# Optimization experiments

Hardware: AMD Instinct MI355X
Metric: run time of the kernel (lower is better)

## Reference

```python
import jax, jax.numpy as jnp
import numpy as np

DIM = 768
NH = 12
HD = DIM // NH
MLP = 4 * DIM
EPS = 1e-5


def _ln(x, w, b):
    mu = x.mean(-1, keepdims=True)
    var = ((x - mu) ** 2).mean(-1, keepdims=True)
    return (x - mu) * jax.lax.rsqrt(var + EPS) * w + b


def setup_inputs() -> dict:
    key = jax.random.key(0)
    ks = jax.random.split(key, 12)
    s = 0.02
    return {
        "xq": jax.random.normal(ks[0], (4, 32, 32, DIM), jnp.float32),
        "xkv": jax.random.normal(ks[1], (4, 64, 64, DIM), jnp.float32),
        "norm1_w": jnp.ones((DIM,), jnp.float32),
        "norm1_b": jnp.zeros((DIM,), jnp.float32),
        "kv_w": jax.random.normal(ks[2], (DIM, 2 * DIM), jnp.float32) * s,
        "kv_b": jnp.zeros((2 * DIM,), jnp.float32),
        "q_w": jax.random.normal(ks[3], (DIM, DIM), jnp.float32) * s,
        "q_b": jnp.zeros((DIM,), jnp.float32),
        "proj_w": jax.random.normal(ks[4], (DIM, DIM), jnp.float32) * s,
        "proj_b": jnp.zeros((DIM,), jnp.float32),
        "norm2_w": jnp.ones((DIM,), jnp.float32),
        "norm2_b": jnp.zeros((DIM,), jnp.float32),
        "mlp_w1": jax.random.normal(ks[5], (DIM, MLP), jnp.float32) * s,
        "mlp_b1": jnp.zeros((MLP,), jnp.float32),
        "mlp_w2": jax.random.normal(ks[6], (MLP, DIM), jnp.float32) * s,
        "mlp_b2": jnp.zeros((DIM,), jnp.float32),
    }


def reference(xq, xkv, norm1_w, norm1_b, kv_w, kv_b, q_w, q_b, proj_w, proj_b,
              norm2_w, norm2_b, mlp_w1, mlp_b1, mlp_w2, mlp_b2):
    B, Hq, Wq, C = xq.shape
    _, H, W, _ = xkv.shape
    shortcut = xq
    xn = _ln(xq, norm1_w, norm1_b)
    # kv projection: [B, H*W, 2, NH, HD]
    kv = (xkv.reshape(B, H * W, C) @ kv_w + kv_b).reshape(B, H * W, 2, NH, HD)
    k = kv[:, :, 0].transpose(0, 2, 1, 3)  # [B, NH, HW, HD]
    v = kv[:, :, 1].transpose(0, 2, 1, 3)
    q = (xn.reshape(B, Hq * Wq, C) @ q_w + q_b).reshape(B, Hq * Wq, NH, HD).transpose(0, 2, 1, 3)
    scale = HD ** -0.5
    attn = jnp.einsum('bhqd,bhkd->bhqk', q * scale, k)
    attn = jax.nn.softmax(attn, axis=-1)
    o = jnp.einsum('bhqk,bhkd->bhqd', attn, v)  # [B, NH, HqWq, HD]
    o = o.transpose(0, 2, 1, 3).reshape(B, Hq, Wq, C)
    o = o @ proj_w + proj_b
    x = shortcut + o
    xn2 = _ln(x, norm2_w, norm2_b)
    mlp = jax.nn.gelu(xn2 @ mlp_w1 + mlp_b1, approximate=False) @ mlp_w2 + mlp_b2
    return x + mlp
```

## Files before the change

kernel.cpp:

```cpp
#include <hip/hip_runtime.h>
#include <hip/hip_bf16.h>
#include <math.h>

#define DIM 768
#define NH 12
#define HD 64
#define NQ 1024
#define NKV 4096
#define QSCALE 0.18033688011112042f

typedef __attribute__((ext_vector_type(4))) float f32x4;
typedef __attribute__((ext_vector_type(8))) __bf16 bf16x8;
typedef __attribute__((ext_vector_type(8))) unsigned short u16x8;
typedef __attribute__((ext_vector_type(4))) unsigned short u16x4;
typedef unsigned short u16;

typedef const __attribute__((address_space(1))) void* gas_t;
typedef __attribute__((address_space(3))) void* las_t;

__device__ __forceinline__ void gl16(const void* g, void* l) {
    __builtin_amdgcn_global_load_lds((gas_t)g, (las_t)l, 16, 0, 0);
}

__device__ __forceinline__ u16 f2b(float x) {
    __bf16 h = (__bf16)x;
    return __builtin_bit_cast(u16, h);
}

__device__ __forceinline__ float b2f(u16 x) {
    unsigned int u = ((unsigned int)x) << 16;
    return __builtin_bit_cast(float, u);
}

__device__ __forceinline__ f32x4 mfma16(const u16* a, const u16* b, f32x4 c) {
    bf16x8 av = *reinterpret_cast<const bf16x8*>(a);
    bf16x8 bv = *reinterpret_cast<const bf16x8*>(b);
    return __builtin_amdgcn_mfma_f32_16x16x32_bf16(av, bv, c, 0, 0, 0);
}

__device__ __forceinline__ f32x4 mfmaf(bf16x8 a, bf16x8 b, f32x4 c) {
    return __builtin_amdgcn_mfma_f32_16x16x32_bf16(a, b, c, 0, 0, 0);
}

__device__ __forceinline__ bf16x8 cat44(u16x4 a, u16x4 b) {
    u16x8 r = __builtin_shufflevector(a, b, 0, 1, 2, 3, 4, 5, 6, 7);
    return __builtin_bit_cast(bf16x8, r);
}

__global__ __launch_bounds__(256) void cast_bf16_kernel(
    const float* __restrict__ in, u16* __restrict__ out, int n8)
{
    int i = blockIdx.x * 256 + threadIdx.x;
    if (i >= n8) return;
    const float4* p = reinterpret_cast<const float4*>(in) + (size_t)i * 2;
    float4 a = p[0], b = p[1];
    u16x8 o;
    o[0] = f2b(a.x); o[1] = f2b(a.y); o[2] = f2b(a.z); o[3] = f2b(a.w);
    o[4] = f2b(b.x); o[5] = f2b(b.y); o[6] = f2b(b.z); o[7] = f2b(b.w);
    reinterpret_cast<u16x8*>(out)[i] = o;
}

__global__ __launch_bounds__(256) void transpose_cast_kernel(
    const float* __restrict__ W, u16* __restrict__ Wt, int K, int N)
{
    __shared__ u16 T[64][72];
    int k0 = blockIdx.y * 64, n0 = blockIdx.x * 64;
    int tid = threadIdx.x;
    int r = tid >> 2, c = (tid & 3) * 16;
    const float* src = W + (size_t)(k0 + r) * N + n0 + c;
    #pragma unroll
    for (int j = 0; j < 16; j += 4) {
        float4 f = *reinterpret_cast<const float4*>(src + j);
        T[r][c + j + 0] = f2b(f.x); T[r][c + j + 1] = f2b(f.y);
        T[r][c + j + 2] = f2b(f.z); T[r][c + j + 3] = f2b(f.w);
    }
    __syncthreads();
    int d = tid >> 2, c2 = (tid & 3) * 16;
    u16x8 o0, o1;
    #pragma unroll
    for (int j = 0; j < 8; ++j) o0[j] = T[c2 + j][d];
    #pragma unroll
    for (int j = 0; j < 8; ++j) o1[j] = T[c2 + 8 + j][d];
    u16* dst = Wt + (size_t)(n0 + d) * K + k0 + c2;
    *reinterpret_cast<u16x8*>(dst) = o0;
    *reinterpret_cast<u16x8*>(dst + 8) = o1;
}

__global__ __launch_bounds__(256) void ln_kernel(
    const float* __restrict__ x, const float* __restrict__ w,
    const float* __restrict__ b, u16* __restrict__ out)
{
    int row = blockIdx.x;
    const float* xr = x + (size_t)row * DIM;
    int tid = threadIdx.x;
    float v0 = xr[tid], v1 = xr[tid + 256], v2 = xr[tid + 512];
    float s = v0 + v1 + v2;
    float s2 = v0 * v0 + v1 * v1 + v2 * v2;
    for (int off = 1; off < 64; off <<= 1) {
        s += __shfl_xor(s, off);
        s2 += __shfl_xor(s2, off);
    }
    __shared__ float ss[4], ss2[4];
    int wid = tid >> 6, lane = tid & 63;
    if (lane == 0) { ss[wid] = s; ss2[wid] = s2; }
    __syncthreads();
    s = ss[0] + ss[1] + ss[2] + ss[3];
    s2 = ss2[0] + ss2[1] + ss2[2] + ss2[3];
    float mu = s * (1.0f / DIM);
    float var = s2 * (1.0f / DIM) - mu * mu;
    float r = rsqrtf(var + 1e-5f);
    u16* orow = out + (size_t)row * DIM;
    orow[tid]       = f2b((v0 - mu) * r * w[tid]       + b[tid]);
    orow[tid + 256] = f2b((v1 - mu) * r * w[tid + 256] + b[tid + 256]);
    orow[tid + 512] = f2b((v2 - mu) * r * w[tid + 512] + b[tid + 512]);
}

template <int EPI>
__global__ __launch_bounds__(256) void gemm_kernel(
    const u16* __restrict__ A, const u16* __restrict__ Bt,
    const float* __restrict__ bias, const float* __restrict__ res,
    void* __restrict__ out, void* __restrict__ out2, int M, int N, int K)
{
    __shared__ u16 As[2][4096];
    __shared__ u16 Bs[2][4096];
    int p = blockIdx.x;
    int nbx = N >> 7;
    int ypx = (M >> 7) >> 3;
    int xcd = p & 7, slot = p >> 3;
    int by = xcd * ypx + slot / nbx;
    int bx = slot - (slot / nbx) * nbx;
    int n0 = bx * 128, m0 = by * 128;
    int tid = threadIdx.x, lane = tid & 63, wave = tid >> 6;
    int wm = (wave >> 1) * 64, wn = (wave & 1) * 64;
    f32x4 acc[4][4] = {};

    int ca = tid, cb = tid + 256;
    int ra = ca >> 2, sa = ((ca & 3) ^ (ra & 3)) * 8;
    int rb = cb >> 2, sb = ((cb & 3) ^ (rb & 3)) * 8;
    const u16* Asrc1 = A + (size_t)(m0 + ra) * K + sa;
    const u16* Asrc2 = A + (size_t)(m0 + rb) * K + sb;
    const u16* Bsrc1 = Bt + (size_t)(n0 + ra) * K + sa;
    const u16* Bsrc2 = Bt + (size_t)(n0 + rb) * K + sb;

    auto STAGE = [&](int buf, int k0) {
        gl16(Asrc1 + k0, &As[buf][ca * 8]);
        gl16(Asrc2 + k0, &As[buf][cb * 8]);
        gl16(Bsrc1 + k0, &Bs[buf][ca * 8]);
        gl16(Bsrc2 + k0, &Bs[buf][cb * 8]);
    };

    int fr = lane & 15, fq = lane >> 4;
    int co = (fq ^ (fr & 3)) * 8;

    auto COMPUTE = [&](int buf) {
        #pragma unroll
        for (int mf = 0; mf < 4; ++mf) {
            const u16* a = &As[buf][(wm + mf * 16 + fr) * 32 + co];
            #pragma unroll
            for (int nf = 0; nf < 4; ++nf)
                acc[mf][nf] = mfma16(a, &Bs[buf][(wn + nf * 16 + fr) * 32 + co],
                                     acc[mf][nf]);
        }
    };

    STAGE(0, 0);
    asm volatile("s_waitcnt vmcnt(0)" ::: "memory");
    __builtin_amdgcn_s_barrier();
    for (int k0 = 0; k0 < K; k0 += 64) {
        STAGE(1, k0 + 32);
        COMPUTE(0);
        asm volatile("s_waitcnt vmcnt(0)" ::: "memory");
        __builtin_amdgcn_s_barrier();
        if (k0 + 64 < K) STAGE(0, k0 + 64);
        COMPUTE(1);
        asm volatile("s_waitcnt vmcnt(0)" ::: "memory");
        __builtin_amdgcn_s_barrier();
    }

    if constexpr (EPI == 4) {
        u16* kb = reinterpret_cast<u16*>(out);
        u16* vtb = reinterpret_cast<u16*>(out2);
        if (n0 < 768) {
            #pragma unroll
            for (int mf = 0; mf < 4; ++mf)
                #pragma unroll
                for (int nf = 0; nf < 4; ++nf) {
                    int col = n0 + wn + nf * 16 + fr;
                    float bv = bias[col];
                    #pragma unroll
                    for (int r = 0; r < 4; ++r) {
                        int row = m0 + wm + mf * 16 + fq * 4 + r;
                        kb[(size_t)row * 768 + col] = f2b(acc[mf][nf][r] + bv);
                    }
                }
        } else {
            #pragma unroll
            for (int mf = 0; mf < 4; ++mf)
                #pragma unroll
                for (int nf = 0; nf < 4; ++nf) {
                    int col = n0 + wn + nf * 16 + fr;
                    int c = col - 768, h = c >> 6, d = c & 63;
                    float bv = bias[col];
                    int row0 = m0 + wm + mf * 16 + fq * 4;
                    int bb = row0 >> 12, kvi = row0 & 4095;
                    int slot = (kvi & 32) | ((kvi & 12) << 1) | ((kvi & 16) >> 2);
                    u16x4 pv;
                    #pragma unroll
                    for (int r = 0; r < 4; ++r) pv[r] = f2b(acc[mf][nf][r] + bv);
                    *reinterpret_cast<u16x4*>(vtb + ((size_t)(bb * 12 + h) * 64 + d) * 4096
                                              + (kvi & ~63) + slot) = pv;
                }
        }
        return;
    }

    float* outf = reinterpret_cast<float*>(out);
    u16* outb = reinterpret_cast<u16*>(out);
    #pragma unroll
    for (int mf = 0; mf < 4; ++mf)
        #pragma unroll
        for (int nf = 0; nf < 4; ++nf)
            #pragma unroll
            for (int r = 0; r < 4; ++r) {
                int row = m0 + wm + mf * 16 + fq * 4 + r;
                int col = n0 + wn + nf * 16 + fr;
                size_t idx = (size_t)row * N + col;
                float v = acc[mf][nf][r] + bias[col];
                if constexpr (EPI == 1) {
                    outb[idx] = f2b(v * QSCALE);
                } else if constexpr (EPI == 2) {
                    outf[idx] = v + res[idx];
                } else {
                    float g = 0.5f * v * (1.0f + erff(v * 0.70710678118f));
                    outb[idx] = f2b(g);
                }
            }
}

__global__ __launch_bounds__(256, 4) void attn_kernel(
    const u16* __restrict__ q, const u16* __restrict__ kbuf,
    const u16* __restrict__ vt, u16* __restrict__ op0, u16* __restrict__ op1,
    float* __restrict__ L)
{
    int p = blockIdx.x;
    int xcd = p & 7, slot = p >> 3;
    int bh = xcd * 6 + (slot >> 5);
    int rem = slot & 31;
    int qt = rem >> 1, half = rem & 1;
    int h = bh % NH, bb = bh / NH;
    const int NIT = 32;

    __shared__ u16 Kb[2][4096];
    __shared__ u16 Vb[2][4096];
    __shared__ float lrow[64];

    int tid = threadIdx.x, lane = tid & 63, wave = tid >> 6;
    int fr = lane & 15, fq = lane >> 4;
    int dd = fr & 7;

    bf16x8 qf[2];
    {
        const u16* qb = q + (size_t)(bb * NQ + qt * 64 + wave * 16 + fr) * DIM + h * HD + fq * 8;
        qf[0] = *reinterpret_cast<const bf16x8*>(qb);
        qf[1] = *reinterpret_cast<const bf16x8*>(qb + 32);
    }

    int c1 = tid, c2 = tid + 256;
    int r1 = c1 >> 3, sc1 = (c1 & 7) ^ (r1 & 7);
    int r2 = c2 >> 3, sc2 = (c2 & 7) ^ (r2 & 7);
    size_t krow0 = (size_t)bb * NKV + half * 2048;
    const u16* ks1 = kbuf + (krow0 + r1) * 768 + h * HD + sc1 * 8;
    const u16* ks2 = kbuf + (krow0 + r2) * 768 + h * HD + sc2 * 8;
    const u16* vs1 = vt + ((size_t)bh * HD + r1) * NKV + half * 2048 + sc1 * 8;
    const u16* vs2 = vt + ((size_t)bh * HD + r2) * NKV + half * 2048 + sc2 * 8;

    auto STAGE = [&](int buf, int kv0) {
        gl16(ks1 + (size_t)kv0 * 768, &Kb[buf][c1 * 8]);
        gl16(ks2 + (size_t)kv0 * 768, &Kb[buf][c2 * 8]);
        gl16(vs1 + kv0, &Vb[buf][c1 * 8]);
        gl16(vs2 + kv0, &Vb[buf][c2 * 8]);
    };

    f32x4 oacc[4] = {};
    float lacc = 0.f;

    STAGE(0, 0);
    asm volatile("s_waitcnt vmcnt(0)" ::: "memory");
    __builtin_amdgcn_s_barrier();

    int kc0 = (fq ^ dd) * 8;
    int kc1 = ((4 + fq) ^ dd) * 8;

    auto BODY = [&](int cur, int it) {
        if (it + 1 < NIT) STAGE(cur ^ 1, (it + 1) * 64);
        const u16* kb = &Kb[cur][fr * 64];
        const u16* vb = &Vb[cur][fr * 64];
        f32x4 s[4] = {};
        #pragma unroll
        for (int mf = 0; mf < 4; ++mf) {
            bf16x8 k0 = *reinterpret_cast<const bf16x8*>(kb + mf * 1024 + kc0);
            bf16x8 k1 = *reinterpret_cast<const bf16x8*>(kb + mf * 1024 + kc1);
            s[mf] = mfmaf(k0, qf[0], s[mf]);
            s[mf] = mfmaf(k1, qf[1], s[mf]);
        }
        float sum = 0.f;
        u16x4 pw[4];
        #pragma unroll
        for (int mf = 0; mf < 4; ++mf) {
            float e0 = exp2f(s[mf][0]), e1 = exp2f(s[mf][1]);
            float e2 = exp2f(s[mf][2]), e3 = exp2f(s[mf][3]);
            sum += (e0 + e1) + (e2 + e3);
            pw[mf][0] = f2b(e0); pw[mf][1] = f2b(e1);
            pw[mf][2] = f2b(e2); pw[mf][3] = f2b(e3);
        }
        sum += __shfl_xor(sum, 16);
        sum += __shfl_xor(sum, 32);
        lacc += sum;
        bf16x8 a1 = cat44(pw[0], pw[1]);
        bf16x8 a2 = cat44(pw[2], pw[3]);
        #pragma unroll
        for (int dt = 0; dt < 4; ++dt) {
            bf16x8 b1 = *reinterpret_cast<const bf16x8*>(vb + dt * 1024 + kc0);
            bf16x8 b2 = *reinterpret_cast<const bf16x8*>(vb + dt * 1024 + kc1);
            oacc[dt] = mfmaf(a1, b1, oacc[dt]);
            oacc[dt] = mfmaf(a2, b2, oacc[dt]);
        }
        asm volatile("s_waitcnt vmcnt(0)" ::: "memory");
        __builtin_amdgcn_s_barrier();
    };

    for (int it = 0; it < NIT; it += 2) { BODY(0, it); BODY(1, it + 1); }

    if (fq == 0) lrow[wave * 16 + fr] = lacc;
    __syncthreads();
    if (fq == 0) L[half * 49152 + bh * 1024 + qt * 64 + wave * 16 + fr] = lacc;
    u16* op = half ? op1 : op0;
    #pragma unroll
    for (int dt = 0; dt < 4; ++dt)
        #pragma unroll
        for (int r = 0; r < 4; ++r) {
            int row = wave * 16 + fq * 4 + r;
            float v = oacc[dt][r] / lrow[row];
            op[(size_t)(bb * NQ + qt * 64 + row) * DIM + h * HD + dt * 16 + fr] = f2b(v);
        }
}

__global__ __launch_bounds__(256) void combine_kernel(
    const u16* __restrict__ op0, const u16* __restrict__ op1,
    const float* __restrict__ L, u16* __restrict__ out)
{
    int idx = blockIdx.x * 256 + threadIdx.x;
    int t = idx / 96, cc = (idx - t * 96) * 8;
    int h = cc >> 6;
    int bb = t >> 10, qr = t & 1023;
    int li = (bb * 12 + h) * 1024 + qr;
    float l0 = L[li], l1 = L[49152 + li];
    float w0 = l0 / (l0 + l1), w1 = 1.0f - w0;
    u16x8 a = *reinterpret_cast<const u16x8*>(op0 + (size_t)t * 768 + cc);
    u16x8 b = *reinterpret_cast<const u16x8*>(op1 + (size_t)t * 768 + cc);
    u16x8 o;
    #pragma unroll
    for (int j = 0; j < 8; ++j) o[j] = f2b(b2f(a[j]) * w0 + b2f(b[j]) * w1);
    *reinterpret_cast<u16x8*>(out + (size_t)t * 768 + cc) = o;
}

extern "C" void kernel_launch(void* const* d_in, const int* in_sizes, int n_in,
                              void* d_out, int out_size, void* d_ws, size_t ws_size,
                              hipStream_t stream) {
    const float* xq  = (const float*)d_in[0];
    const float* xkv = (const float*)d_in[1];
    const float* n1w = (const float*)d_in[2];
    const float* n1b = (const float*)d_in[3];
    const float* kvw = (const float*)d_in[4];
    const float* kvb = (const float*)d_in[5];
    const float* qw  = (const float*)d_in[6];
    const float* qb  = (const float*)d_in[7];
    const float* pjw = (const float*)d_in[8];
    const float* pjb = (const float*)d_in[9];
    const float* n2w = (const float*)d_in[10];
    const float* n2b = (const float*)d_in[11];
    const float* w1  = (const float*)d_in[12];
    const float* b1  = (const float*)d_in[13];
    const float* w2  = (const float*)d_in[14];
    const float* b2  = (const float*)d_in[15];
    float* xout = (float*)d_out;

    char* ws = (char*)d_ws;
    u16* xkv_b  = (u16*)(ws);
    u16* kbuf   = (u16*)(ws + 25165824);
    u16* vt     = (u16*)(ws + 50331648);
    u16* xn_bf  = (u16*)(ws + 75497472);
    u16* q_bf   = (u16*)(ws + 81788928);
    u16* o_bf   = (u16*)(ws + 88080384);
    u16* wkv_bf = (u16*)(ws + 94371840);
    u16* wq_bf  = (u16*)(ws + 96731136);
    u16* wpj_bf = (u16*)(ws + 97910784);
    u16* w1_bf  = (u16*)(ws + 99090432);
    u16* w2_bf  = (u16*)(ws + 103809024);
    u16* hid    = xkv_b;
    float* Lbuf = (float*)wkv_bf;

    cast_bf16_kernel<<<dim3(6144), dim3(256), 0, stream>>>(xkv, xkv_b, 1572864);
    transpose_cast_kernel<<<dim3(24, 12), dim3(256), 0, stream>>>(kvw, wkv_bf, 768, 1536);
    transpose_cast_kernel<<<dim3(12, 12), dim3(256), 0, stream>>>(qw, wq_bf, 768, 768);
    transpose_cast_kernel<<<dim3(12, 12), dim3(256), 0, stream>>>(pjw, wpj_bf, 768, 768);
    transpose_cast_kernel<<<dim3(48, 12), dim3(256), 0, stream>>>(w1, w1_bf, 768, 3072);
    transpose_cast_kernel<<<dim3(12, 48), dim3(256), 0, stream>>>(w2, w2_bf, 3072, 768);

    ln_kernel<<<dim3(4096), dim3(256), 0, stream>>>(xq, n1w, n1b, xn_bf);
    gemm_kernel<4><<<dim3(12 * 128), dim3(256), 0, stream>>>(xkv_b, wkv_bf, kvb, nullptr, kbuf, vt, 16384, 1536, 768);
    gemm_kernel<1><<<dim3(6 * 32), dim3(256), 0, stream>>>(xn_bf, wq_bf, qb, nullptr, q_bf, nullptr, 4096, 768, 768);
    attn_kernel<<<dim3(1536), dim3(256), 0, stream>>>(q_bf, kbuf, vt, xn_bf, o_bf, Lbuf);
    combine_kernel<<<dim3(1536), dim3(256), 0, stream>>>(xn_bf, o_bf, Lbuf, q_bf);
    gemm_kernel<2><<<dim3(6 * 32), dim3(256), 0, stream>>>(q_bf, wpj_bf, pjb, xq, xout, nullptr, 4096, 768, 768);
    ln_kernel<<<dim3(4096), dim3(256), 0, stream>>>(xout, n2w, n2b, xn_bf);
    gemm_kernel<3><<<dim3(24 * 32), dim3(256), 0, stream>>>(xn_bf, w1_bf, b1, nullptr, hid, nullptr, 4096, 3072, 768);
    gemm_kernel<2><<<dim3(6 * 32), dim3(256), 0, stream>>>(hid, w2_bf, b2, xout, xout, nullptr, 4096, 768, 3072);
}
```

Before: 335.5 us.

## Add 64x64-tile GEMM for narrow projections and compute softmax sums via MFMA

Adds a 64x64-tile GEMM kernel for the q, proj and MLP-down projections (N=768), raising the grid from 192 to 768 blocks so all CUs get work. In attention, the per-row exp sums are accumulated with an MFMA against a ones vector instead of shuffles, and the LDS row buffer and its barrier are removed. The smaller tiles reuse each loaded tile less and use fewer MFMAs per load, and the sum now adds bf16-rounded probabilities, which changes rounding slightly.

```diff
diff --git a/kernel.cpp b/kernel.cpp
--- a/kernel.cpp
+++ b/kernel.cpp
@@ -226,13 +226,90 @@
                 int col = n0 + wn + nf * 16 + fr;
                 size_t idx = (size_t)row * N + col;
                 float v = acc[mf][nf][r] + bias[col];
-                if constexpr (EPI == 1) {
-                    outb[idx] = f2b(v * QSCALE);
-                } else if constexpr (EPI == 2) {
+                if constexpr (EPI == 2) {
                     outf[idx] = v + res[idx];
                 } else {
                     float g = 0.5f * v * (1.0f + erff(v * 0.70710678118f));
                     outb[idx] = f2b(g);
+                }
+            }
+}
+
+template <int EPI>
+__global__ __launch_bounds__(256) void gemm64_kernel(
+    const u16* __restrict__ A, const u16* __restrict__ Bt,
+    const float* __restrict__ bias, const float* __restrict__ res,
+    void* __restrict__ out, int M, int N, int K)
+{
+    __shared__ u16 As[2][4096];
+    __shared__ u16 Bs[2][4096];
+    int p = blockIdx.x;
+    int nbx = N >> 6;
+    int ypx = (M >> 6) >> 3;
+    int xcd = p & 7, slot = p >> 3;
+    int by = xcd * ypx + slot / nbx;
+    int bx = slot - (slot / nbx) * nbx;
+    int n0 = bx * 64, m0 = by * 64;
+    int tid = threadIdx.x, lane = tid & 63, wave = tid >> 6;
+    int wm = (wave >> 1) * 32, wn = (wave & 1) * 32;
+    f32x4 acc[2][2] = {};
+
+    int c1 = tid, c2 = tid + 256;
+    int r1 = c1 >> 3, s1 = ((c1 & 7) ^ (r1 & 7)) * 8;
+    int r2 = c2 >> 3, s2 = ((c2 & 7) ^ (r2 & 7)) * 8;
+    const u16* As1 = A + (size_t)(m0 + r1) * K + s1;
+    const u16* As2 = A + (size_t)(m0 + r2) * K + s2;
+    const u16* Bt1 = Bt + (size_t)(n0 + r1) * K + s1;
+    const u16* Bt2 = Bt + (size_t)(n0 + r2) * K + s2;
+
+    auto STAGE = [&](int buf, int k0) {
+        gl16(As1 + k0, &As[buf][c1 * 8]);
+        gl16(As2 + k0, &As[buf][c2 * 8]);
+        gl16(Bt1 + k0, &Bs[buf][c1 * 8]);
+        gl16(Bt2 + k0, &Bs[buf][c2 * 8]);
+    };
+
+    int fr = lane & 15, fq = lane >> 4;
+    int co0 = (fq ^ (fr & 7)) * 8;
+    int co1 = ((4 + fq) ^ (fr & 7)) * 8;
+
+    STAGE(0, 0);
+    asm volatile("s_waitcnt vmcnt(0)" ::: "memory");
+    __builtin_amdgcn_s_barrier();
+    int NIT = K >> 6;
+    for (int it = 0; it < NIT; ++it) {
+        int cur = it & 1;
+        if (it + 1 < NIT) STAGE(cur ^ 1, (it + 1) << 6);
+        #pragma unroll
+        for (int mf = 0; mf < 2; ++mf) {
+            const u16* arow = &As[cur][(wm + mf * 16 + fr) * 64];
+            #pragma unroll
+            for (int nf = 0; nf < 2; ++nf) {
+                const u16* brow = &Bs[cur][(wn + nf * 16 + fr) * 64];
+                acc[mf][nf] = mfma16(arow + co0, brow + co0, acc[mf][nf]);
+                acc[mf][nf] = mfma16(arow + co1, brow + co1, acc[mf][nf]);
+            }
+        }
+        asm volatile("s_waitcnt vmcnt(0)" ::: "memory");
+        __builtin_amdgcn_s_barrier();
+    }
+
+    float* outf = reinterpret_cast<float*>(out);
+    u16* outb = reinterpret_cast<u16*>(out);
+    #pragma unroll
+    for (int mf = 0; mf < 2; ++mf)
+        #pragma unroll
+        for (int nf = 0; nf < 2; ++nf)
+            #pragma unroll
+            for (int r = 0; r < 4; ++r) {
+                int row = m0 + wm + mf * 16 + fq * 4 + r;
+                int col = n0 + wn + nf * 16 + fr;
+                size_t idx = (size_t)row * N + col;
+                float v = acc[mf][nf][r] + bias[col];
+                if constexpr (EPI == 1) {
+                    outb[idx] = f2b(v * QSCALE);
+                } else {
+                    outf[idx] = v + res[idx];
                 }
             }
 }
@@ -252,11 +329,13 @@
 
     __shared__ u16 Kb[2][4096];
     __shared__ u16 Vb[2][4096];
-    __shared__ float lrow[64];
 
     int tid = threadIdx.x, lane = tid & 63, wave = tid >> 6;
     int fr = lane & 15, fq = lane >> 4;
     int dd = fr & 7;
+
+    u16x8 ov = {0x3F80, 0x3F80, 0x3F80, 0x3F80, 0x3F80, 0x3F80, 0x3F80, 0x3F80};
+    const bf16x8 ONES = __builtin_bit_cast(bf16x8, ov);
 
     bf16x8 qf[2];
     {
@@ -282,7 +361,7 @@
     };
 
     f32x4 oacc[4] = {};
-    float lacc = 0.f;
+    f32x4 lsum = {};
 
     STAGE(0, 0);
     asm volatile("s_waitcnt vmcnt(0)" ::: "memory");
@@ -303,21 +382,18 @@
             s[mf] = mfmaf(k0, qf[0], s[mf]);
             s[mf] = mfmaf(k1, qf[1], s[mf]);
         }
-        float sum = 0.f;
         u16x4 pw[4];
         #pragma unroll
         for (int mf = 0; mf < 4; ++mf) {
-            float e0 = exp2f(s[mf][0]), e1 = exp2f(s[mf][1]);
-            float e2 = exp2f(s[mf][2]), e3 = exp2f(s[mf][3]);
-            sum += (e0 + e1) + (e2 + e3);
-            pw[mf][0] = f2b(e0); pw[mf][1] = f2b(e1);
-            pw[mf][2] = f2b(e2); pw[mf][3] = f2b(e3);
-        }
-        sum += __shfl_xor(sum, 16);
-        sum += __shfl_xor(sum, 32);
-        lacc += sum;
+            pw[mf][0] = f2b(exp2f(s[mf][0]));
+            pw[mf][1] = f2b(exp2f(s[mf][1]));
+            pw[mf][2] = f2b(exp2f(s[mf][2]));
+            pw[mf][3] = f2b(exp2f(s[mf][3]));
+        }
         bf16x8 a1 = cat44(pw[0], pw[1]);
         bf16x8 a2 = cat44(pw[2], pw[3]);
+        lsum = mfmaf(a1, ONES, lsum);
+        lsum = mfmaf(a2, ONES, lsum);
         #pragma unroll
         for (int dt = 0; dt < 4; ++dt) {
             bf16x8 b1 = *reinterpret_cast<const bf16x8*>(vb + dt * 1024 + kc0);
@@ -331,16 +407,18 @@
 
     for (int it = 0; it < NIT; it += 2) { BODY(0, it); BODY(1, it + 1); }
 
-    if (fq == 0) lrow[wave * 16 + fr] = lacc;
-    __syncthreads();
-    if (fq == 0) L[half * 49152 + bh * 1024 + qt * 64 + wave * 16 + fr] = lacc;
+    if (fr == 0) {
+        #pragma unroll
+        for (int r = 0; r < 4; ++r)
+            L[half * 49152 + bh * 1024 + qt * 64 + wave * 16 + fq * 4 + r] = lsum[r];
+    }
     u16* op = half ? op1 : op0;
     #pragma unroll
     for (int dt = 0; dt < 4; ++dt)
         #pragma unroll
         for (int r = 0; r < 4; ++r) {
             int row = wave * 16 + fq * 4 + r;
-            float v = oacc[dt][r] / lrow[row];
+            float v = oacc[dt][r] / lsum[r];
             op[(size_t)(bb * NQ + qt * 64 + row) * DIM + h * HD + dt * 16 + fr] = f2b(v);
         }
 }
@@ -409,11 +487,11 @@
 
     ln_kernel<<<dim3(4096), dim3(256), 0, stream>>>(xq, n1w, n1b, xn_bf);
     gemm_kernel<4><<<dim3(12 * 128), dim3(256), 0, stream>>>(xkv_b, wkv_bf, kvb, nullptr, kbuf, vt, 16384, 1536, 768);
-    gemm_kernel<1><<<dim3(6 * 32), dim3(256), 0, stream>>>(xn_bf, wq_bf, qb, nullptr, q_bf, nullptr, 4096, 768, 768);
+    gemm64_kernel<1><<<dim3(768), dim3(256), 0, stream>>>(xn_bf, wq_bf, qb, nullptr, q_bf, 4096, 768, 768);
     attn_kernel<<<dim3(1536), dim3(256), 0, stream>>>(q_bf, kbuf, vt, xn_bf, o_bf, Lbuf);
     combine_kernel<<<dim3(1536), dim3(256), 0, stream>>>(xn_bf, o_bf, Lbuf, q_bf);
-    gemm_kernel<2><<<dim3(6 * 32), dim3(256), 0, stream>>>(q_bf, wpj_bf, pjb, xq, xout, nullptr, 4096, 768, 768);
+    gemm64_kernel<2><<<dim3(768), dim3(256), 0, stream>>>(q_bf, wpj_bf, pjb, xq, xout, 4096, 768, 768);
     ln_kernel<<<dim3(4096), dim3(256), 0, stream>>>(xout, n2w, n2b, xn_bf);
     gemm_kernel<3><<<dim3(24 * 32), dim3(256), 0, stream>>>(xn_bf, w1_bf, b1, nullptr, hid, nullptr, 4096, 3072, 768);
-    gemm_kernel<2><<<dim3(6 * 32), dim3(256), 0, stream>>>(hid, w2_bf, b2, xout, xout, nullptr, 4096, 768, 3072);
-}
+    gemm64_kernel<2><<<dim3(768), dim3(256), 0, stream>>>(hid, w2_bf, b2, xout, xout, 4096, 768, 3072);
+}
```

Measured after the change: 289.0 us. 13.9% less time.
